# Optimization experiments

Measured on AMD Instinct MI355X. Metric: run time of the kernel, lower is better.

## Reference

```python
import jax, jax.numpy as jnp
import numpy as np

NOISE_DIM = 128
IN_FEATURES = 512
OUT_FEATURES = 512
BATCH = 256


def setup_inputs() -> dict:
    key = jax.random.key(0)
    k1, k2, k3 = jax.random.split(key, 3)
    out_dim = IN_FEATURES * OUT_FEATURES + OUT_FEATURES
    # x = [noise | features]
    x = jax.random.normal(k1, (BATCH, NOISE_DIM + IN_FEATURES), dtype=jnp.float32)
    # hypermodel Linear params; scale ~ 1/sqrt(fan_in) like torch default init
    scale = 1.0 / np.sqrt(NOISE_DIM)
    W = jax.random.uniform(k2, (NOISE_DIM, out_dim), dtype=jnp.float32, minval=-scale, maxval=scale)
    b = jax.random.uniform(k3, (out_dim,), dtype=jnp.float32, minval=-scale, maxval=scale)
    return {"x": x, "W": W, "b": b}


def reference(x, W, b):
    # split input into hypernet noise and features
    noise = x[:, :NOISE_DIM]            # [B, noise_dim]
    feats = x[:, NOISE_DIM:]            # [B, in_features]
    # hypermodel: generate per-sample linear params
    params = noise @ W + b              # [B, in*out + out]
    w_flat = params[:, : IN_FEATURES * OUT_FEATURES]
    bias = params[:, IN_FEATURES * OUT_FEATURES :]        # [B, out]
    weight = w_flat.reshape(-1, IN_FEATURES, OUT_FEATURES)  # [B, in, out]
    # batched matmul (torch.bmm of [B,1,in] @ [B,in,out]) + bias, squeeze
    out = jnp.einsum("bi,bio->bo", feats, weight) + bias   # [B, out]
    return out
```

## Files before the change

kernel.cpp:

```cpp
#include <hip/hip_runtime.h>
#include <hip/hip_bf16.h>
#include <stdint.h>

namespace {
constexpr int kBatch = 256;
constexpr int kNoise = 128;
constexpr int kIn    = 512;
constexpr int kOut   = 512;
constexpr int kXCols = kNoise + kIn;
constexpr int kPCols = kIn * kOut + kOut;
constexpr int kOTile = 32;
constexpr int kITile = 16;
constexpr int kWStride = 68;
constexpr int kFeatsStride = 260;
}

typedef __bf16 bf16x8 __attribute__((ext_vector_type(8)));
typedef float  f32x4  __attribute__((ext_vector_type(4)));
typedef unsigned int u32x4 __attribute__((ext_vector_type(4)));

__device__ inline unsigned int pack_bf16x2(float lo, float hi) {
    unsigned int a = (unsigned int)__builtin_bit_cast(unsigned short, (__bf16)lo);
    unsigned int b = (unsigned int)__builtin_bit_cast(unsigned short, (__bf16)hi);
    return a | (b << 16);
}

__device__ inline void wg_barrier_lds() {
    __asm__ volatile("" ::: "memory");
    __builtin_amdgcn_s_waitcnt(0xC07F);
    __builtin_amdgcn_s_barrier();
    __asm__ volatile("" ::: "memory");
}

__global__ __launch_bounds__(512, 4)
void hyper_gemm_kernel(const float* __restrict__ x,
                       const float* __restrict__ W,
                       const float* __restrict__ bvec,
                       float* __restrict__ out)
{
    const int tid  = threadIdx.x;
    const int lane = tid & 63;
    const int wave = tid >> 6;
    const int q    = lane >> 4;
    const int l16  = lane & 15;

    const int o0 = blockIdx.x * kOTile;
    const int i0 = blockIdx.y * kITile;

    const int u    = tid >> 3;
    const int colg = (tid & 7) * 4;

    __shared__ unsigned int wtile[kOTile * kWStride];
    __shared__ float feats_lds[kITile * kFeatsStride];

    {
        const int i    = tid & 15;
        const int brow = tid >> 4;
        #pragma unroll
        for (int rep = 0; rep < 8; ++rep) {
            const int b = brow + rep * 32;
            feats_lds[i * kFeatsStride + b] = x[b * kXCols + kNoise + i0 + i];
        }
    }

    bf16x8 afrag[2][4];
    {
        #pragma unroll
        for (int mt = 0; mt < 2; ++mt) {
            const float* xr = x + (size_t)(wave * 32 + mt * 16 + l16) * kXCols;
            #pragma unroll
            for (int s = 0; s < 4; ++s) {
                const float* p = xr + s * 32 + q * 8;
                f32x4 u0 = *(const f32x4*)(p);
                f32x4 u1 = *(const f32x4*)(p + 4);
                bf16x8 a;
                a[0] = (__bf16)u0[0]; a[1] = (__bf16)u0[1];
                a[2] = (__bf16)u0[2]; a[3] = (__bf16)u0[3];
                a[4] = (__bf16)u1[0]; a[5] = (__bf16)u1[1];
                a[6] = (__bf16)u1[2]; a[7] = (__bf16)u1[3];
                afrag[mt][s] = a;
            }
        }
    }

    float oacc[2][2][4];
    #pragma unroll
    for (int mt = 0; mt < 2; ++mt)
        #pragma unroll
        for (int nt = 0; nt < 2; ++nt)
            #pragma unroll
            for (int r = 0; r < 4; ++r) oacc[mt][nt][r] = 0.f;

    __syncthreads();

    const int nPass = (blockIdx.y == 0) ? (kITile + 1) : kITile;

    auto pass_cbase = [&](int p) -> int {
        return (p == kITile) ? (kIn * kOut) : (i0 + p) * kOut;
    };

    f32x4 pr0, pr1;
    {
        const float* wp = W + (size_t)(2 * u) * kPCols + pass_cbase(0) + o0 + colg;
        pr0 = *(const f32x4*)wp;
        pr1 = *(const f32x4*)(wp + kPCols);
    }

    for (int ip = 0; ip < nPass; ++ip) {
        const int cbase = pass_cbase(ip);

        unsigned int pk[4];
        #pragma unroll
        for (int cc = 0; cc < 4; ++cc) pk[cc] = pack_bf16x2(pr0[cc], pr1[cc]);

        wg_barrier_lds();
        #pragma unroll
        for (int cc = 0; cc < 4; ++cc)
            wtile[(colg + cc) * kWStride + u] = pk[cc];

        if (ip + 1 < nPass) {
            const float* wp = W + (size_t)(2 * u) * kPCols + pass_cbase(ip + 1) + o0 + colg;
            pr0 = *(const f32x4*)wp;
            pr1 = *(const f32x4*)(wp + kPCols);
        }

        wg_barrier_lds();

        f32x4 acc[2][2];
        const f32x4 zero = {0.f, 0.f, 0.f, 0.f};
        #pragma unroll
        for (int mt = 0; mt < 2; ++mt)
            #pragma unroll
            for (int nt = 0; nt < 2; ++nt) acc[mt][nt] = zero;

        #pragma unroll
        for (int s = 0; s < 4; ++s) {
            #pragma unroll
            for (int nt = 0; nt < 2; ++nt) {
                u32x4 raw = *(const u32x4*)&wtile[(nt * 16 + l16) * kWStride + s * 16 + q * 4];
                bf16x8 bfrag = __builtin_bit_cast(bf16x8, raw);
                #pragma unroll
                for (int mt = 0; mt < 2; ++mt)
                    acc[mt][nt] = __builtin_amdgcn_mfma_f32_16x16x32_bf16(
                        afrag[mt][s], bfrag, acc[mt][nt], 0, 0, 0);
            }
        }

        const float bv0 = bvec[cbase + o0 + l16];
        const float bv1 = bvec[cbase + o0 + 16 + l16];

        if (ip < kITile) {
            #pragma unroll
            for (int mt = 0; mt < 2; ++mt) {
                const f32x4 f4 = *(const f32x4*)&feats_lds[ip * kFeatsStride
                                        + wave * 32 + mt * 16 + q * 4];
                #pragma unroll
                for (int r = 0; r < 4; ++r) {
                    oacc[mt][0][r] += f4[r] * (acc[mt][0][r] + bv0);
                    oacc[mt][1][r] += f4[r] * (acc[mt][1][r] + bv1);
                }
            }
        } else {
            #pragma unroll
            for (int mt = 0; mt < 2; ++mt)
                #pragma unroll
                for (int r = 0; r < 4; ++r) {
                    oacc[mt][0][r] += acc[mt][0][r] + bv0;
                    oacc[mt][1][r] += acc[mt][1][r] + bv1;
                }
        }
    }

    #pragma unroll
    for (int mt = 0; mt < 2; ++mt)
        #pragma unroll
        for (int nt = 0; nt < 2; ++nt) {
            const int o = o0 + nt * 16 + l16;
            #pragma unroll
            for (int r = 0; r < 4; ++r) {
                const int b = wave * 32 + mt * 16 + q * 4 + r;
                atomicAdd(&out[b * kOut + o], oacc[mt][nt][r]);
            }
        }
}

extern "C" void kernel_launch(void* const* d_in, const int* in_sizes, int n_in,
                              void* d_out, int out_size, void* d_ws, size_t ws_size,
                              hipStream_t stream) {
    const float* x  = (const float*)d_in[0];
    const float* W  = (const float*)d_in[1];
    const float* bv = (const float*)d_in[2];
    float* out = (float*)d_out;

    hipMemsetAsync(out, 0, (size_t)kBatch * kOut * sizeof(float), stream);

    dim3 grid(kOut / kOTile, kIn / kITile);
    hyper_gemm_kernel<<<grid, 512, 0, stream>>>(x, W, bv, out);
}
```

Measured before the change: 215.7 us.

## Double-buffer weight tile, prefetch two passes ahead, replace atomics with split reduction

The weight tile in LDS is double-buffered and global loads are prefetched two passes ahead, which removes one barrier per pass and hides more load latency. Bias values are staged in LDS up front instead of being read from global memory on every pass. The atomicAdd epilogue and the memset are replaced by plain stores of per-split partial sums into workspace, followed by a separate reduce kernel over the 32 splits. This adds 16 MB of partial-sum traffic and an extra kernel launch.

```diff
diff --git a/kernel.cpp b/kernel.cpp
--- a/kernel.cpp
+++ b/kernel.cpp
@@ -11,6 +11,7 @@
 constexpr int kPCols = kIn * kOut + kOut;
 constexpr int kOTile = 32;
 constexpr int kITile = 16;
+constexpr int kSplits = kIn / kITile;
 constexpr int kWStride = 68;
 constexpr int kFeatsStride = 260;
 }
@@ -36,7 +37,7 @@
 void hyper_gemm_kernel(const float* __restrict__ x,
                        const float* __restrict__ W,
                        const float* __restrict__ bvec,
-                       float* __restrict__ out)
+                       float* __restrict__ part)
 {
     const int tid  = threadIdx.x;
     const int lane = tid & 63;
@@ -50,8 +51,28 @@
     const int u    = tid >> 3;
     const int colg = (tid & 7) * 4;
 
-    __shared__ unsigned int wtile[kOTile * kWStride];
+    __shared__ unsigned int wtile[2][kOTile * kWStride];
     __shared__ float feats_lds[kITile * kFeatsStride];
+    __shared__ float bv_lds[(kITile + 1) * kOTile];
+
+    const int nPass = (blockIdx.y == 0) ? (kITile + 1) : kITile;
+
+    auto pass_cbase = [&](int p) -> size_t {
+        return (p == kITile) ? (size_t)(kIn * kOut) : (size_t)(i0 + p) * kOut;
+    };
+    auto wrow = [&](int p) -> const float* {
+        return W + (size_t)(2 * u) * kPCols + pass_cbase(p) + o0 + colg;
+    };
+
+    f32x4 pa0, pa1, pb0, pb1;
+    { const float* wp = wrow(0); pa0 = *(const f32x4*)wp; pa1 = *(const f32x4*)(wp + kPCols); }
+    { const float* wp = wrow(1); pb0 = *(const f32x4*)wp; pb1 = *(const f32x4*)(wp + kPCols); }
+
+    for (int idx = tid; idx < (kITile + 1) * kOTile; idx += 512) {
+        const int p = idx >> 5, c = idx & 31;
+        const size_t cb = (p == kITile) ? (size_t)(kIn * kOut) : (size_t)(i0 + p) * kOut;
+        bv_lds[idx] = bvec[cb + o0 + c];
+    }
 
     {
         const int i    = tid & 15;
@@ -93,35 +114,20 @@
 
     __syncthreads();
 
-    const int nPass = (blockIdx.y == 0) ? (kITile + 1) : kITile;
-
-    auto pass_cbase = [&](int p) -> int {
-        return (p == kITile) ? (kIn * kOut) : (i0 + p) * kOut;
-    };
-
-    f32x4 pr0, pr1;
-    {
-        const float* wp = W + (size_t)(2 * u) * kPCols + pass_cbase(0) + o0 + colg;
-        pr0 = *(const f32x4*)wp;
-        pr1 = *(const f32x4*)(wp + kPCols);
-    }
-
     for (int ip = 0; ip < nPass; ++ip) {
-        const int cbase = pass_cbase(ip);
-
         unsigned int pk[4];
         #pragma unroll
-        for (int cc = 0; cc < 4; ++cc) pk[cc] = pack_bf16x2(pr0[cc], pr1[cc]);
-
-        wg_barrier_lds();
+        for (int cc = 0; cc < 4; ++cc) pk[cc] = pack_bf16x2(pa0[cc], pa1[cc]);
+
+        unsigned int* wt = &wtile[ip & 1][0];
         #pragma unroll
         for (int cc = 0; cc < 4; ++cc)
-            wtile[(colg + cc) * kWStride + u] = pk[cc];
-
-        if (ip + 1 < nPass) {
-            const float* wp = W + (size_t)(2 * u) * kPCols + pass_cbase(ip + 1) + o0 + colg;
-            pr0 = *(const f32x4*)wp;
-            pr1 = *(const f32x4*)(wp + kPCols);
+            wt[(colg + cc) * kWStride + u] = pk[cc];
+
+        pa0 = pb0; pa1 = pb1;
+        if (ip + 2 < nPass) {
+            const float* wp = wrow(ip + 2);
+            pb0 = *(const f32x4*)wp; pb1 = *(const f32x4*)(wp + kPCols);
         }
 
         wg_barrier_lds();
@@ -137,7 +143,7 @@
         for (int s = 0; s < 4; ++s) {
             #pragma unroll
             for (int nt = 0; nt < 2; ++nt) {
-                u32x4 raw = *(const u32x4*)&wtile[(nt * 16 + l16) * kWStride + s * 16 + q * 4];
+                u32x4 raw = *(const u32x4*)&wt[(nt * 16 + l16) * kWStride + s * 16 + q * 4];
                 bf16x8 bfrag = __builtin_bit_cast(bf16x8, raw);
                 #pragma unroll
                 for (int mt = 0; mt < 2; ++mt)
@@ -146,8 +152,8 @@
             }
         }
 
-        const float bv0 = bvec[cbase + o0 + l16];
-        const float bv1 = bvec[cbase + o0 + 16 + l16];
+        const float bv0 = bv_lds[ip * kOTile + l16];
+        const float bv1 = bv_lds[ip * kOTile + 16 + l16];
 
         if (ip < kITile) {
             #pragma unroll
@@ -171,6 +177,7 @@
         }
     }
 
+    float* pp = part + (size_t)blockIdx.y * kBatch * kOut;
     #pragma unroll
     for (int mt = 0; mt < 2; ++mt)
         #pragma unroll
@@ -179,9 +186,20 @@
             #pragma unroll
             for (int r = 0; r < 4; ++r) {
                 const int b = wave * 32 + mt * 16 + q * 4 + r;
-                atomicAdd(&out[b * kOut + o], oacc[mt][nt][r]);
-            }
-        }
+                pp[(size_t)b * kOut + o] = oacc[mt][nt][r];
+            }
+        }
+}
+
+__global__ __launch_bounds__(256)
+void reduce_kernel(const float* __restrict__ part, float* __restrict__ out)
+{
+    const size_t idx4 = ((size_t)blockIdx.x * 256 + threadIdx.x) * 4;
+    f32x4 acc = *(const f32x4*)(part + idx4);
+    #pragma unroll
+    for (int s = 1; s < kSplits; ++s)
+        acc += *(const f32x4*)(part + (size_t)s * kBatch * kOut + idx4);
+    *(f32x4*)(out + idx4) = acc;
 }
 
 extern "C" void kernel_launch(void* const* d_in, const int* in_sizes, int n_in,
@@ -190,10 +208,12 @@
     const float* x  = (const float*)d_in[0];
     const float* W  = (const float*)d_in[1];
     const float* bv = (const float*)d_in[2];
-    float* out = (float*)d_out;
-
-    hipMemsetAsync(out, 0, (size_t)kBatch * kOut * sizeof(float), stream);
-
-    dim3 grid(kOut / kOTile, kIn / kITile);
-    hyper_gemm_kernel<<<grid, 512, 0, stream>>>(x, W, bv, out);
-}
+    float* out  = (float*)d_out;
+    float* part = (float*)d_ws;
+
+    dim3 grid(kOut / kOTile, kSplits);
+    hyper_gemm_kernel<<<grid, 512, 0, stream>>>(x, W, bv, part);
+
+    const int n4 = kBatch * kOut / 4;
+    reduce_kernel<<<n4 / 256, 256, 0, stream>>>(part, out);
+}
```

After: 217.6 us. Within noise of the previous version (+0.9%).
